# Kernel optimization log

Measured on AMD Instinct MI355X. Metric: run time of the kernel, lower is better.

## Reference

```python
import jax, jax.numpy as jnp
import numpy as np

S, R, CM, CZ, H = 128, 256, 256, 128, 8
HD = CM // H
INF = 1e9
EPS = 1e-5


def _ln(x, g, b):
    mu = jnp.mean(x, axis=-1, keepdims=True)
    var = jnp.var(x, axis=-1, keepdims=True)
    return (x - mu) * jax.lax.rsqrt(var + EPS) * g + b


def setup_inputs() -> dict:
    key = jax.random.key(0)
    ks = jax.random.split(key, 12)
    d = {
        'm': jax.random.normal(ks[0], (S, R, CM), jnp.float32),
        'z': jax.random.normal(ks[1], (R, R, CZ), jnp.float32),
        'mask': jnp.ones((S, R), jnp.float32),
        'ln_m_g': jnp.ones((CM,), jnp.float32),
        'ln_m_b': jnp.zeros((CM,), jnp.float32),
        'ln_z_g': jnp.ones((CZ,), jnp.float32),
        'ln_z_b': jnp.zeros((CZ,), jnp.float32),
        'w_z': jax.random.normal(ks[2], (CZ, H), jnp.float32) * 0.02,
        'wq': jax.random.normal(ks[3], (CM, CM), jnp.float32) * (1.0 / np.sqrt(CM)),
        'wk': jax.random.normal(ks[4], (CM, CM), jnp.float32) * (1.0 / np.sqrt(CM)),
        'wv': jax.random.normal(ks[5], (CM, CM), jnp.float32) * (1.0 / np.sqrt(CM)),
        'wg': jnp.zeros((CM, CM), jnp.float32),
        'bg': jnp.ones((CM,), jnp.float32),
        'wo': jax.random.normal(ks[6], (CM, CM), jnp.float32) * (1.0 / np.sqrt(CM)),
        'bo': jnp.zeros((CM,), jnp.float32),
    }
    return d


def reference(m, z, mask, ln_m_g, ln_m_b, ln_z_g, ln_z_b, w_z, wq, wk, wv, wg, bg, wo, bo):
    # pair bias: LN(z) -> per-head bias [H, R, R], broadcast over seq rows
    z_ln = _ln(z, ln_z_g, ln_z_b)
    pair_bias = jnp.einsum('ijc,ch->hij', z_ln, w_z)          # [H, R, R]
    mask_bias = (INF * (mask - 1.0))[:, None, None, :]        # [S, 1, 1, R]

    m_ln = _ln(m, ln_m_g, ln_m_b)                             # [S, R, CM]
    q = (m_ln @ wq).reshape(S, R, H, HD)
    k = (m_ln @ wk).reshape(S, R, H, HD)
    v = (m_ln @ wv).reshape(S, R, H, HD)

    scale = 1.0 / np.sqrt(HD).astype(np.float32)
    logits = jnp.einsum('sihd,sjhd->shij', q * scale, k)       # [S, H, R, R]
    logits = logits + pair_bias[None] + mask_bias
    attn = jax.nn.softmax(logits, axis=-1)

    o = jnp.einsum('shij,sjhd->sihd', attn, v).reshape(S, R, CM)
    g = jax.nn.sigmoid(m_ln @ wg + bg)
    return (g * o) @ wo + bo
```

## Files before the change

kernel.cpp:

```cpp
#include <hip/hip_runtime.h>
#include <hip/hip_bf16.h>

typedef unsigned short u16;
typedef __bf16 bf16x8 __attribute__((ext_vector_type(8)));
typedef float f32x4 __attribute__((ext_vector_type(4)));
typedef float f32x16 __attribute__((ext_vector_type(16)));
typedef unsigned short u16x8 __attribute__((ext_vector_type(8)));
typedef unsigned short u16x4 __attribute__((ext_vector_type(4)));

#define LOG2E 1.4426950408889634f

__device__ __forceinline__ u16 f2b(float f) {
  union { __bf16 b; u16 u; } v; v.b = (__bf16)f; return v.u;
}
__device__ __forceinline__ float bf2f(u16 u) {
  union { unsigned u; float f; } v; v.u = ((unsigned)u) << 16;
  return v.f;
}
__device__ __forceinline__ float fexp2(float x) {
  return __builtin_amdgcn_exp2f(x);
}
__device__ __forceinline__ void pinv(f32x4& v) {
  asm volatile("" : "+v"(v));
}

__global__ __launch_bounds__(256) void k_pre(
    const float* __restrict__ wq, const float* __restrict__ wk,
    const float* __restrict__ wv, const float* __restrict__ wg,
    const float* __restrict__ wo, u16* __restrict__ wtp,
    const float* __restrict__ z, const float* __restrict__ zg,
    const float* __restrict__ zb, const float* __restrict__ wz,
    float* __restrict__ pbp,
    const float* __restrict__ m, const float* __restrict__ gam,
    const float* __restrict__ bet, u16* __restrict__ mlp) {
  __shared__ float lt[64][68];
  const int b = blockIdx.x;
  const int t = threadIdx.x;
  if (b < 80) {
    const int widx = b >> 4;
    const int tid = b & 15;
    const int ri = (tid >> 2) * 64, ci = (tid & 3) * 64;
    const float* src = (widx == 0) ? wq : (widx == 1) ? wk : (widx == 2) ? wv
                      : (widx == 3) ? wg : wo;
    {
      const int r = t >> 2;
      #pragma unroll
      for (int i = 0; i < 4; ++i) {
        const int c = (t & 3) * 16 + i * 4;
        *(float4*)&lt[r][c] = *(const float4*)&src[(ri + r) * 256 + ci + c];
      }
    }
    __syncthreads();
    #pragma unroll
    for (int cc = 0; cc < 2; ++cc) {
      const int c = t + cc * 256;
      const int kb = c >> 8, cb = (c >> 6) & 3, lg = (c >> 4) & 3, lr = c & 15;
      u16x8 o;
      #pragma unroll
      for (int j = 0; j < 8; ++j) o[j] = f2b(lt[kb * 32 + lg * 8 + j][cb * 16 + lr]);
      const size_t idx = (size_t)widx * 65536 + (size_t)((ci >> 4) + cb) * 4096
                       + (size_t)((ri >> 5) + kb) * 512 + (size_t)(lg * 16 + lr) * 8;
      *(u16x8*)&wtp[idx] = o;
    }
  } else if (b < 4176) {
    const int lane = t & 63, wave = t >> 6;
    const int ql = lane & 15;
    const int p = (b - 80) * 16 + wave * 4 + (lane >> 4);
    const float4 zv0 = *(const float4*)(z + (size_t)p * 128 + ql * 8);
    const float4 zv1 = *(const float4*)(z + (size_t)p * 128 + ql * 8 + 4);
    float s = zv0.x + zv0.y + zv0.z + zv0.w + zv1.x + zv1.y + zv1.z + zv1.w;
    float sq = zv0.x * zv0.x + zv0.y * zv0.y + zv0.z * zv0.z + zv0.w * zv0.w
             + zv1.x * zv1.x + zv1.y * zv1.y + zv1.z * zv1.z + zv1.w * zv1.w;
    #pragma unroll
    for (int o = 8; o > 0; o >>= 1) { s += __shfl_xor(s, o); sq += __shfl_xor(sq, o); }
    const float mu = s * 0.0078125f;
    const float var = sq * 0.0078125f - mu * mu;
    const float rs = rsqrtf(var + 1e-5f);
    const int c0 = ql * 8;
    float zn[8];
    zn[0] = (zv0.x - mu) * rs * zg[c0 + 0] + zb[c0 + 0];
    zn[1] = (zv0.y - mu) * rs * zg[c0 + 1] + zb[c0 + 1];
    zn[2] = (zv0.z - mu) * rs * zg[c0 + 2] + zb[c0 + 2];
    zn[3] = (zv0.w - mu) * rs * zg[c0 + 3] + zb[c0 + 3];
    zn[4] = (zv1.x - mu) * rs * zg[c0 + 4] + zb[c0 + 4];
    zn[5] = (zv1.y - mu) * rs * zg[c0 + 5] + zb[c0 + 5];
    zn[6] = (zv1.z - mu) * rs * zg[c0 + 6] + zb[c0 + 6];
    zn[7] = (zv1.w - mu) * rs * zg[c0 + 7] + zb[c0 + 7];
    float a[8] = {};
    #pragma unroll
    for (int i = 0; i < 8; ++i) {
      #pragma unroll
      for (int hh = 0; hh < 8; ++hh) a[hh] += zn[i] * wz[(c0 + i) * 8 + hh];
    }
    #pragma unroll
    for (int hh = 0; hh < 8; ++hh) {
      #pragma unroll
      for (int o = 8; o > 0; o >>= 1) a[hh] += __shfl_xor(a[hh], o);
    }
    if (ql == 0) {
      const int i = p >> 8, j = p & 255;
      const int strip = i >> 5, il = i & 31, jt = j >> 5, r = j & 31;
      const int gh = (r >> 2) & 1, qd = r >> 3, c4 = r & 3;
      const int off = (strip * 8 + jt) * 1024 + (gh * 32 + il) * 16 + qd * 4 + c4;
      #pragma unroll
      for (int hh = 0; hh < 8; ++hh)
        pbp[(size_t)hh * 65536 + off] = a[hh] * LOG2E;
    }
  } else {
    const int lane = t & 63;
    const size_t row = (size_t)(b - 4176) * 4 + (t >> 6);
    const float4 xv = *(const float4*)(m + row * 256 + lane * 4);
    float s = xv.x + xv.y + xv.z + xv.w;
    float sq = xv.x * xv.x + xv.y * xv.y + xv.z * xv.z + xv.w * xv.w;
    #pragma unroll
    for (int o = 32; o > 0; o >>= 1) { s += __shfl_xor(s, o); sq += __shfl_xor(sq, o); }
    const float mu = s * 0.00390625f;
    const float var = sq * 0.00390625f - mu * mu;
    const float rs = rsqrtf(var + 1e-5f);
    const int c = lane * 4;
    u16x4 o4;
    o4.x = f2b((xv.x - mu) * rs * gam[c] + bet[c]);
    o4.y = f2b((xv.y - mu) * rs * gam[c + 1] + bet[c + 1]);
    o4.z = f2b((xv.z - mu) * rs * gam[c + 2] + bet[c + 2]);
    o4.w = f2b((xv.w - mu) * rs * gam[c + 3] + bet[c + 3]);
    const size_t ss = row >> 8;
    const int rloc = (int)(row & 255);
    const int ch = rloc >> 5, il = rloc & 31;
    const size_t dst = ss * 65536 + (size_t)ch * 8192 + (size_t)(lane >> 2) * 512
                     + (size_t)(((lane >> 1) & 1) * 32 + il) * 8 + (lane & 1) * 4;
    *(u16x4*)&mlp[dst] = o4;
  }
}

__global__ __launch_bounds__(256, 3) void k_fused(
    const u16* __restrict__ mlp, const u16* __restrict__ wtp,
    const float* __restrict__ bg, const float* __restrict__ pbp,
    const float* __restrict__ mask, u16* __restrict__ g,
    u16* __restrict__ go) {
  __shared__ u16 lQ[256 * 32];
  __shared__ u16 lK[256 * 32];
  __shared__ u16 lVt[32][276];
  __shared__ float lMb[256];
  __shared__ float lL[4][32];
  const int bid = blockIdx.x;
  const int s = bid & 127, h = bid >> 7;
  const int t = threadIdx.x;
  const int lane = t & 63, wave = t >> 6;
  const int il = lane & 31, gh = lane >> 5;

  const u16* Wb = wtp + (size_t)wave * 65536 + (size_t)(2 * h + (il >> 4)) * 4096
                + gh * 128 + (il & 15) * 8;
  bf16x8 B[16];
  #pragma unroll
  for (int kc = 0; kc < 16; ++kc) B[kc] = *(const bf16x8*)&Wb[kc * 256];
  #pragma unroll
  for (int kc = 0; kc < 16; ++kc) pinv(*reinterpret_cast<f32x4*>(&B[kc]));

  lMb[t] = (LOG2E * 1e9f) * (mask[s * 256 + t] - 1.0f) - 24.0f;
  const float bgv = bg[h * 32 + il];
  const u16* Ab = mlp + (size_t)s * 65536 + (size_t)lane * 8;

  #pragma unroll
  for (int c = 0; c < 8; ++c) {
    f32x16 a0 = {}, a1 = {};
    bf16x8 A0[8];
    #pragma unroll
    for (int kc = 0; kc < 8; ++kc)
      A0[kc] = *(const bf16x8*)&Ab[c * 8192 + kc * 512];
    #pragma unroll
    for (int kc = 0; kc < 8; kc += 2) {
      a0 = __builtin_amdgcn_mfma_f32_32x32x16_bf16(A0[kc], B[kc], a0, 0, 0, 0);
      a1 = __builtin_amdgcn_mfma_f32_32x32x16_bf16(A0[kc + 1], B[kc + 1], a1, 0, 0, 0);
    }
    bf16x8 A1[8];
    #pragma unroll
    for (int kc = 0; kc < 8; ++kc)
      A1[kc] = *(const bf16x8*)&Ab[c * 8192 + (kc + 8) * 512];
    #pragma unroll
    for (int kc = 0; kc < 8; kc += 2) {
      a0 = __builtin_amdgcn_mfma_f32_32x32x16_bf16(A1[kc], B[kc + 8], a0, 0, 0, 0);
      a1 = __builtin_amdgcn_mfma_f32_32x32x16_bf16(A1[kc + 1], B[kc + 9], a1, 0, 0, 0);
    }
    const f32x16 acc = a0 + a1;
    if (wave == 0) {
      #pragma unroll
      for (int reg = 0; reg < 16; ++reg) {
        const int R = c * 32 + (reg & 3) + 8 * (reg >> 2) + 4 * gh;
        *(u16*)((char*)lQ + ((R * 64 + il * 2) ^ ((R & 7) << 4))) =
            f2b(acc[reg] * (0.17677669529663687f * LOG2E));
      }
    } else if (wave == 1) {
      #pragma unroll
      for (int reg = 0; reg < 16; ++reg) {
        const int R = c * 32 + (reg & 3) + 8 * (reg >> 2) + 4 * gh;
        *(u16*)((char*)lK + ((R * 64 + il * 2) ^ ((R & 7) << 4))) = f2b(acc[reg]);
      }
    } else if (wave == 2) {
      #pragma unroll
      for (int reg = 0; reg < 16; ++reg) {
        const int R = c * 32 + (reg & 3) + 8 * (reg >> 2) + 4 * gh;
        lVt[il][R] = f2b(acc[reg]);
      }
    } else {
      #pragma unroll
      for (int reg = 0; reg < 16; ++reg) {
        const int R = c * 32 + (reg & 3) + 8 * (reg >> 2) + 4 * gh;
        const float x = acc[reg] + bgv;
        g[(size_t)(s * 256 + R) * 256 + h * 32 + il] =
            f2b(1.0f / (1.0f + __expf(-x)));
      }
    }
  }
  __syncthreads();

  #pragma unroll 1
  for (int strip = 0; strip < 2; ++strip) {
    const int i0 = wave * 64 + strip * 32;
    bf16x8 qf[2];
    #pragma unroll
    for (int kk = 0; kk < 2; ++kk) {
      const int row = i0 + il;
      qf[kk] = *(const bf16x8*)((const char*)lQ +
          ((row * 64 + (kk * 16 + gh * 8) * 2) ^ ((row & 7) << 4)));
    }
    const float* pbt = pbp + ((size_t)h * 8 + (i0 >> 5)) * 8192 + lane * 16;

    f32x16 oacc0 = {}, oacc1 = {};
    float s0 = 0.f, s1 = 0.f, s2 = 0.f, s3 = 0.f;

    #pragma unroll 2
    for (int jt = 0; jt < 8; ++jt) {
      const float* pl = pbt + jt * 1024;
      f32x16 c;
      #pragma unroll
      for (int qd = 0; qd < 4; ++qd) {
        const f32x4 pbq = *(const f32x4*)&pl[qd * 4];
        const f32x4 mb4 = *(const f32x4*)&lMb[jt * 32 + qd * 8 + gh * 4];
        #pragma unroll
        for (int c4 = 0; c4 < 4; ++c4)
          c[qd * 4 + c4] = pbq[c4] + mb4[c4];
      }
      const int krow = jt * 32 + il;
      const bf16x8 kf0 = *(const bf16x8*)((const char*)lK +
          ((krow * 64 + (gh * 8) * 2) ^ ((krow & 7) << 4)));
      const bf16x8 kf1 = *(const bf16x8*)((const char*)lK +
          ((krow * 64 + (16 + gh * 8) * 2) ^ ((krow & 7) << 4)));
      c = __builtin_amdgcn_mfma_f32_32x32x16_bf16(kf0, qf[0], c, 0, 0, 0);
      c = __builtin_amdgcn_mfma_f32_32x32x16_bf16(kf1, qf[1], c, 0, 0, 0);
      union PK { __bf16 h[4]; uint2 u; } pk[4];
      #pragma unroll
      for (int qd = 0; qd < 4; ++qd) {
        const float p0 = fexp2(c[qd * 4 + 0]);
        const float p1 = fexp2(c[qd * 4 + 1]);
        const float p2 = fexp2(c[qd * 4 + 2]);
        const float p3 = fexp2(c[qd * 4 + 3]);
        s0 += p0; s1 += p1; s2 += p2; s3 += p3;
        pk[qd].h[0] = (__bf16)p0; pk[qd].h[1] = (__bf16)p1;
        pk[qd].h[2] = (__bf16)p2; pk[qd].h[3] = (__bf16)p3;
      }
      const uint2 sA = gh ? pk[0].u : pk[1].u;
      uint2 rA; rA.x = __shfl_xor(sA.x, 32); rA.y = __shfl_xor(sA.y, 32);
      const uint2 sB = gh ? pk[2].u : pk[3].u;
      uint2 rB; rB.x = __shfl_xor(sB.x, 32); rB.y = __shfl_xor(sB.y, 32);
      union FR { uint2 u2[2]; bf16x8 v; } fa0, fa1;
      fa0.u2[0] = gh ? rA : pk[0].u;
      fa0.u2[1] = gh ? pk[1].u : rA;
      fa1.u2[0] = gh ? rB : pk[2].u;
      fa1.u2[1] = gh ? pk[3].u : rB;
      const bf16x8 vf0 = *(const bf16x8*)&lVt[il][jt * 32 + gh * 8];
      const bf16x8 vf1 = *(const bf16x8*)&lVt[il][jt * 32 + 16 + gh * 8];
      oacc0 = __builtin_amdgcn_mfma_f32_32x32x16_bf16(fa0.v, vf0, oacc0, 0, 0, 0);
      oacc1 = __builtin_amdgcn_mfma_f32_32x32x16_bf16(fa1.v, vf1, oacc1, 0, 0, 0);
    }

    float lsum = (s0 + s1) + (s2 + s3);
    lsum += __shfl_xor(lsum, 32);
    if (lane < 32) lL[wave][il] = 1.0f / lsum;

    #pragma unroll
    for (int qd = 0; qd < 4; ++qd) {
      const f32x4 invq = *(const f32x4*)&lL[wave][qd * 8 + gh * 4];
      #pragma unroll
      for (int c4 = 0; c4 < 4; ++c4) {
        const int iloc = qd * 8 + gh * 4 + c4;
        const size_t row = (size_t)s * 256 + i0 + iloc;
        const int col = h * 32 + il;
        const float ov = (oacc0[qd * 4 + c4] + oacc1[qd * 4 + c4]) * invq[c4];
        const float gv = bf2f(g[row * 256 + col]);
        go[row * 256 + col] = f2b(gv * ov);
      }
    }
  }
}

__global__ __launch_bounds__(256, 4) void k_gemm_out(
    const u16* __restrict__ go, const u16* __restrict__ wop,
    const float* __restrict__ bo, float* __restrict__ out) {
  __shared__ u16 lA[32 * 256];
  const int t = threadIdx.x;
  const size_t row0 = (size_t)blockIdx.x * 32;
  const int lane = t & 63, wave = t >> 6;
  const u16* Wz = wop + (size_t)wave * 16384 + (size_t)lane * 8;
  u16x8 areg[4];
  #pragma unroll
  for (int i = 0; i < 4; ++i)
    areg[i] = *(const u16x8*)&go[(row0 + i * 8 + (t >> 5)) * 256 + (t & 31) * 8];
  bf16x8 B[4][4];
  #pragma unroll
  for (int kc = 0; kc < 4; ++kc) {
    #pragma unroll
    for (int nn = 0; nn < 4; ++nn)
      B[kc][nn] = *(const bf16x8*)&Wz[nn * 4096 + kc * 512];
  }
  __builtin_amdgcn_sched_barrier(0);
  #pragma unroll
  for (int i = 0; i < 4; ++i) {
    const int r = i * 8 + (t >> 5);
    const int c = (t & 31) * 8;
    *(u16x8*)((char*)lA + ((r * 512 + c * 2) ^ ((r & 7) << 4))) = areg[i];
  }
  __syncthreads();
  const int lrow = lane & 15, lg = lane >> 4;
  f32x4 acc[2][4] = {};
  #pragma unroll
  for (int kc = 0; kc < 4; ++kc) {
    bf16x8 af[2];
    #pragma unroll
    for (int mm = 0; mm < 2; ++mm) {
      const int row = mm * 16 + lrow;
      af[mm] = *(const bf16x8*)((const char*)lA +
          ((row * 512 + kc * 64 + lg * 16) ^ ((row & 7) << 4)));
    }
    #pragma unroll
    for (int mm = 0; mm < 2; ++mm) {
      #pragma unroll
      for (int nn = 0; nn < 4; ++nn)
        acc[mm][nn] = __builtin_amdgcn_mfma_f32_16x16x32_bf16(
            af[mm], B[kc][nn], acc[mm][nn], 0, 0, 0);
    }
  }
  #pragma unroll
  for (int kc = 0; kc < 4; ++kc) {
    #pragma unroll
    for (int nn = 0; nn < 4; ++nn)
      B[kc][nn] = *(const bf16x8*)&Wz[nn * 4096 + (kc + 4) * 512];
  }
  __builtin_amdgcn_sched_barrier(0);
  #pragma unroll
  for (int kc = 0; kc < 4; ++kc) {
    bf16x8 af[2];
    #pragma unroll
    for (int mm = 0; mm < 2; ++mm) {
      const int row = mm * 16 + lrow;
      af[mm] = *(const bf16x8*)((const char*)lA +
          ((row * 512 + (kc + 4) * 64 + lg * 16) ^ ((row & 7) << 4)));
    }
    #pragma unroll
    for (int mm = 0; mm < 2; ++mm) {
      #pragma unroll
      for (int nn = 0; nn < 4; ++nn)
        acc[mm][nn] = __builtin_amdgcn_mfma_f32_16x16x32_bf16(
            af[mm], B[kc][nn], acc[mm][nn], 0, 0, 0);
    }
  }
  const int wc = wave * 64, lg4 = lg * 4;
  #pragma unroll
  for (int mm = 0; mm < 2; ++mm) {
    #pragma unroll
    for (int nn = 0; nn < 4; ++nn) {
      const int col = wc + nn * 16 + lrow;
      #pragma unroll
      for (int jr = 0; jr < 4; ++jr) {
        const size_t row = row0 + mm * 16 + lg4 + jr;
        out[row * 256 + col] = acc[mm][nn][jr] + bo[col];
      }
    }
  }
}

extern "C" void kernel_launch(void* const* d_in, const int* in_sizes, int n_in,
                              void* d_out, int out_size, void* d_ws, size_t ws_size,
                              hipStream_t stream) {
  const float* m      = (const float*)d_in[0];
  const float* z      = (const float*)d_in[1];
  const float* mask   = (const float*)d_in[2];
  const float* ln_m_g = (const float*)d_in[3];
  const float* ln_m_b = (const float*)d_in[4];
  const float* ln_z_g = (const float*)d_in[5];
  const float* ln_z_b = (const float*)d_in[6];
  const float* w_z    = (const float*)d_in[7];
  const float* wq     = (const float*)d_in[8];
  const float* wk     = (const float*)d_in[9];
  const float* wv     = (const float*)d_in[10];
  const float* wg     = (const float*)d_in[11];
  const float* bg     = (const float*)d_in[12];
  const float* wo     = (const float*)d_in[13];
  const float* bo     = (const float*)d_in[14];
  float* out = (float*)d_out;

  char* w = (char*)d_ws;
  u16* wtp   = (u16*)w;   w += (size_t)5 * 65536 * 2;
  float* pbp = (float*)w; w += (size_t)8 * 65536 * 4;
  u16* mlp   = (u16*)w;   w += (size_t)32768 * 256 * 2;
  u16* gow   = (u16*)w;   w += (size_t)32768 * 256 * 2;
  u16* gw    = (u16*)w;   w += (size_t)32768 * 256 * 2;

  k_pre      <<<12368, 256, 0, stream>>>(wq, wk, wv, wg, wo, wtp,
                                         z, ln_z_g, ln_z_b, w_z, pbp,
                                         m, ln_m_g, ln_m_b, mlp);
  k_fused    <<<1024, 256, 0, stream>>>(mlp, wtp, bg, pbp, mask, gw, gow);
  k_gemm_out <<<1024, 256, 0, stream>>>(gow, wtp + (size_t)4 * 65536, bo, out);
}
```

Measured before the change: 122.0 us.

## Double fused attention block to 512 threads and keep gate in LDS

Raises the fused kernel from 4 to 8 waves per block. Each projection (Q, K, V, gate) is now split across two waves by row half, and each wave handles one 32-row attention strip instead of two sequential strips. The sigmoid gate is kept in shared memory instead of being written to and read back from a global buffer. This adds parallelism per block and removes a global round trip. In exchange it uses more LDS per block and doubles the per-block weight-register loads, since each B fragment is now loaded by two waves.

New measurement: 113.1 us (median of 2 runs). 7.3% less time.

```diff
diff --git a/kernel.cpp b/kernel.cpp
--- a/kernel.cpp
+++ b/kernel.cpp
@@ -19,9 +19,6 @@
 }
 __device__ __forceinline__ float fexp2(float x) {
   return __builtin_amdgcn_exp2f(x);
-}
-__device__ __forceinline__ void pinv(f32x4& v) {
-  asm volatile("" : "+v"(v));
 }
 
 __global__ __launch_bounds__(256) void k_pre(
@@ -132,36 +129,37 @@
   }
 }
 
-__global__ __launch_bounds__(256, 3) void k_fused(
+__global__ __launch_bounds__(512, 4) void k_fused(
     const u16* __restrict__ mlp, const u16* __restrict__ wtp,
     const float* __restrict__ bg, const float* __restrict__ pbp,
-    const float* __restrict__ mask, u16* __restrict__ g,
-    u16* __restrict__ go) {
+    const float* __restrict__ mask, u16* __restrict__ go) {
+  __shared__ u16 gP[256 * 32];
   __shared__ u16 lQ[256 * 32];
   __shared__ u16 lK[256 * 32];
   __shared__ u16 lVt[32][276];
   __shared__ float lMb[256];
-  __shared__ float lL[4][32];
+  __shared__ float lL[8][32];
   const int bid = blockIdx.x;
   const int s = bid & 127, h = bid >> 7;
   const int t = threadIdx.x;
   const int lane = t & 63, wave = t >> 6;
   const int il = lane & 31, gh = lane >> 5;
-
-  const u16* Wb = wtp + (size_t)wave * 65536 + (size_t)(2 * h + (il >> 4)) * 4096
+  const int z = wave >> 1, half = wave & 1;
+
+  const u16* Wb = wtp + (size_t)z * 65536 + (size_t)(2 * h + (il >> 4)) * 4096
                 + gh * 128 + (il & 15) * 8;
   bf16x8 B[16];
   #pragma unroll
   for (int kc = 0; kc < 16; ++kc) B[kc] = *(const bf16x8*)&Wb[kc * 256];
-  #pragma unroll
-  for (int kc = 0; kc < 16; ++kc) pinv(*reinterpret_cast<f32x4*>(&B[kc]));
-
-  lMb[t] = (LOG2E * 1e9f) * (mask[s * 256 + t] - 1.0f) - 24.0f;
+
+  if (t < 256)
+    lMb[t] = (LOG2E * 1e9f) * (mask[s * 256 + t] - 1.0f) - 24.0f;
   const float bgv = bg[h * 32 + il];
   const u16* Ab = mlp + (size_t)s * 65536 + (size_t)lane * 8;
 
   #pragma unroll
-  for (int c = 0; c < 8; ++c) {
+  for (int cc = 0; cc < 4; ++cc) {
+    const int c = half * 4 + cc;
     f32x16 a0 = {}, a1 = {};
     bf16x8 A0[8];
     #pragma unroll
@@ -182,20 +180,20 @@
       a1 = __builtin_amdgcn_mfma_f32_32x32x16_bf16(A1[kc + 1], B[kc + 9], a1, 0, 0, 0);
     }
     const f32x16 acc = a0 + a1;
-    if (wave == 0) {
+    if (z == 0) {
       #pragma unroll
       for (int reg = 0; reg < 16; ++reg) {
         const int R = c * 32 + (reg & 3) + 8 * (reg >> 2) + 4 * gh;
         *(u16*)((char*)lQ + ((R * 64 + il * 2) ^ ((R & 7) << 4))) =
             f2b(acc[reg] * (0.17677669529663687f * LOG2E));
       }
-    } else if (wave == 1) {
+    } else if (z == 1) {
       #pragma unroll
       for (int reg = 0; reg < 16; ++reg) {
         const int R = c * 32 + (reg & 3) + 8 * (reg >> 2) + 4 * gh;
         *(u16*)((char*)lK + ((R * 64 + il * 2) ^ ((R & 7) << 4))) = f2b(acc[reg]);
       }
-    } else if (wave == 2) {
+    } else if (z == 2) {
       #pragma unroll
       for (int reg = 0; reg < 16; ++reg) {
         const int R = c * 32 + (reg & 3) + 8 * (reg >> 2) + 4 * gh;
@@ -206,16 +204,14 @@
       for (int reg = 0; reg < 16; ++reg) {
         const int R = c * 32 + (reg & 3) + 8 * (reg >> 2) + 4 * gh;
         const float x = acc[reg] + bgv;
-        g[(size_t)(s * 256 + R) * 256 + h * 32 + il] =
-            f2b(1.0f / (1.0f + __expf(-x)));
+        gP[R * 32 + il] = f2b(1.0f / (1.0f + __expf(-x)));
       }
     }
   }
   __syncthreads();
 
-  #pragma unroll 1
-  for (int strip = 0; strip < 2; ++strip) {
-    const int i0 = wave * 64 + strip * 32;
+  {
+    const int i0 = wave * 32;
     bf16x8 qf[2];
     #pragma unroll
     for (int kk = 0; kk < 2; ++kk) {
@@ -223,7 +219,7 @@
       qf[kk] = *(const bf16x8*)((const char*)lQ +
           ((row * 64 + (kk * 16 + gh * 8) * 2) ^ ((row & 7) << 4)));
     }
-    const float* pbt = pbp + ((size_t)h * 8 + (i0 >> 5)) * 8192 + lane * 16;
+    const float* pbt = pbp + ((size_t)h * 8 + wave) * 8192 + lane * 16;
 
     f32x16 oacc0 = {}, oacc1 = {};
     float s0 = 0.f, s1 = 0.f, s2 = 0.f, s3 = 0.f;
@@ -286,7 +282,7 @@
         const size_t row = (size_t)s * 256 + i0 + iloc;
         const int col = h * 32 + il;
         const float ov = (oacc0[qd * 4 + c4] + oacc1[qd * 4 + c4]) * invq[c4];
-        const float gv = bf2f(g[row * 256 + col]);
+        const float gv = bf2f(gP[(i0 + iloc) * 32 + il]);
         go[row * 256 + col] = f2b(gv * ov);
       }
     }
@@ -403,11 +399,10 @@
   float* pbp = (float*)w; w += (size_t)8 * 65536 * 4;
   u16* mlp   = (u16*)w;   w += (size_t)32768 * 256 * 2;
   u16* gow   = (u16*)w;   w += (size_t)32768 * 256 * 2;
-  u16* gw    = (u16*)w;   w += (size_t)32768 * 256 * 2;
 
   k_pre      <<<12368, 256, 0, stream>>>(wq, wk, wv, wg, wo, wtp,
                                          z, ln_z_g, ln_z_b, w_z, pbp,
                                          m, ln_m_g, ln_m_b, mlp);
-  k_fused    <<<1024, 256, 0, stream>>>(mlp, wtp, bg, pbp, mask, gw, gow);
+  k_fused    <<<1024, 512, 0, stream>>>(mlp, wtp, bg, pbp, mask, gow);
   k_gemm_out <<<1024, 256, 0, stream>>>(gow, wtp + (size_t)4 * 65536, bo, out);
 }
```
